# Performance work log

Measured on AMD Instinct MI355X. Metric: run time of the kernel, lower is better.

Reference implementation:

```python
import jax, jax.numpy as jnp
import numpy as np

B, C, H, W = 8, 256, 128, 128
HEADS = 4
HEAD_DIM = C // HEADS  # 64
SCALE = HEAD_DIM ** -0.5


def setup_inputs() -> dict:
    key = jax.random.key(0)
    k1, k2, k3 = jax.random.split(key, 3)
    x = jax.random.normal(k1, (B, C, H, W), dtype=jnp.float32)
    # 1x1 convs == per-pixel linear layers; kaiming-ish small init
    Wqkv = jax.random.normal(k2, (3 * C, C), dtype=jnp.float32) * (1.0 / np.sqrt(C))
    bqkv = jnp.zeros((3 * C,), dtype=jnp.float32)
    Wproj = jax.random.normal(k3, (C, C), dtype=jnp.float32) * (1.0 / np.sqrt(C))
    bproj = jnp.zeros((C,), dtype=jnp.float32)
    return {"x": x, "Wqkv": Wqkv, "bqkv": bqkv, "Wproj": Wproj, "bproj": bproj}


def reference(x, Wqkv, bqkv, Wproj, bproj):
    b, c, h, w = x.shape
    hw = h * w
    xf = x.reshape(b, c, hw)  # [b, c, hw]
    # 1x1 conv QKV projection
    qkv = jnp.einsum('bcn,oc->bon', xf, Wqkv) + bqkv[None, :, None]  # [b, 3c, hw]
    qkv = qkv.reshape(b, 3, HEADS, HEAD_DIM, hw)
    q, k, v = qkv[:, 0], qkv[:, 1], qkv[:, 2]  # each [b, heads, d, hw]
    # channel attention: [b, heads, d, d]
    attn = jnp.einsum('bhdn,bhen->bhde', q, k) * SCALE
    attn = jax.nn.softmax(attn, axis=-1)
    out = jnp.einsum('bhde,bhen->bhdn', attn, v).reshape(b, c, hw)
    # output 1x1 conv
    out = jnp.einsum('bcn,oc->bon', out, Wproj) + bproj[None, :, None]
    return out.reshape(b, c, h, w)
```

## Files before the change

### kernel.cpp

```cpp
#include <hip/hip_runtime.h>
#include <hip/hip_bf16.h>
#include <stdint.h>


#define HW 16384
#define SCALE_F 0.125f
#define NF 16384.0f

typedef __attribute__((ext_vector_type(8))) short bf16x8;
typedef __attribute__((ext_vector_type(4))) float f32x4;

__device__ __forceinline__ unsigned short f2bf(float f) {
    union { float f; uint32_t u; } v; v.f = f;
    uint32_t u = v.u;
    return (unsigned short)((u + 0x7fffu + ((u >> 16) & 1u)) >> 16);
}
__device__ __forceinline__ float bf2f(unsigned short s) {
    union { uint32_t u; float f; } v; v.u = ((uint32_t)s) << 16;
    return v.f;
}

__global__ __launch_bounds__(512) void gram(
        const float* __restrict__ x, float* __restrict__ partG,
        float* __restrict__ parts_s) {
    const int kc = blockIdx.x;
    const int b  = blockIdx.y;
    __shared__ __align__(16) unsigned short Hs[2][256 * 32];
    __shared__ __align__(16) unsigned short Ls[2][256 * 32];
    const int tid = threadIdx.x, lane = tid & 63, w = tid >> 6;
    const int l15 = lane & 15, lg = lane >> 4;
    const int wr = w >> 1, wc = w & 1;
    const int srow = tid >> 1, shalf = tid & 1;
    const int m4 = (srow >> 1) & 3;
    const float* xb = x + (size_t)b * 256 * HW + (size_t)srow * HW + kc * 512 + shalf * 16;
    f32x4 acc[4][8] = {};
    float rs = 0.f;
    float4 ld[4];

#define LOADR(kstep)                                                            \
    {                                                                           \
        const float4* src = reinterpret_cast<const float4*>(xb + (kstep) * 32); \
        ld[0] = src[0]; ld[1] = src[1]; ld[2] = src[2]; ld[3] = src[3];         \
    }
#define STORE(sel)                                                              \
    {                                                                           \
        _Pragma("unroll")                                                       \
        for (int cq = 0; cq < 2; ++cq) {                                        \
            union { unsigned short u[8]; uint4 v; } Hu, Lu;                     \
            const float vv[8] = {ld[2*cq].x, ld[2*cq].y, ld[2*cq].z, ld[2*cq].w,\
                                 ld[2*cq+1].x, ld[2*cq+1].y, ld[2*cq+1].z, ld[2*cq+1].w}; \
            _Pragma("unroll")                                                   \
            for (int i = 0; i < 8; ++i) {                                       \
                Hu.u[i] = f2bf(vv[i]);                                          \
                Lu.u[i] = f2bf(vv[i] - bf2f(Hu.u[i]));                          \
                rs += vv[i];                                                    \
            }                                                                   \
            const int slot = ((shalf * 2 + cq) ^ m4) << 4;                      \
            *reinterpret_cast<uint4*>((char*)(&Hs[sel][0]) + srow * 64 + slot) = Hu.v; \
            *reinterpret_cast<uint4*>((char*)(&Ls[sel][0]) + srow * 64 + slot) = Lu.v; \
        }                                                                       \
    }
#define DO_MFMA(sel)                                                            \
    {                                                                           \
        bf16x8 fah[4], fal[4];                                                  \
        _Pragma("unroll")                                                       \
        for (int i = 0; i < 4; ++i) {                                           \
            const int row = wr * 64 + i * 16 + l15;                             \
            const int off = row * 64 + ((lg ^ ((row >> 1) & 3)) << 4);          \
            fah[i] = *reinterpret_cast<const bf16x8*>((const char*)&Hs[sel][0] + off); \
            fal[i] = *reinterpret_cast<const bf16x8*>((const char*)&Ls[sel][0] + off); \
        }                                                                       \
        _Pragma("unroll")                                                       \
        for (int j = 0; j < 8; ++j) {                                           \
            const int row = wc * 128 + j * 16 + l15;                            \
            const int off = row * 64 + ((lg ^ ((row >> 1) & 3)) << 4);          \
            const bf16x8 fbh = *reinterpret_cast<const bf16x8*>((const char*)&Hs[sel][0] + off); \
            const bf16x8 fbl = *reinterpret_cast<const bf16x8*>((const char*)&Ls[sel][0] + off); \
            _Pragma("unroll")                                                   \
            for (int i = 0; i < 4; ++i) {                                       \
                acc[i][j] = __builtin_amdgcn_mfma_f32_16x16x32_bf16(fah[i], fbh, acc[i][j], 0, 0, 0); \
                acc[i][j] = __builtin_amdgcn_mfma_f32_16x16x32_bf16(fah[i], fbl, acc[i][j], 0, 0, 0); \
                acc[i][j] = __builtin_amdgcn_mfma_f32_16x16x32_bf16(fal[i], fbh, acc[i][j], 0, 0, 0); \
            }                                                                   \
        }                                                                       \
    }

    LOADR(0);
    STORE(0);
    __syncthreads();
    for (int t = 0; t < 16; ++t) {
        if (t < 15) LOADR(t + 1);
        DO_MFMA(t & 1);
        if (t < 15) STORE((t + 1) & 1);
        __syncthreads();
    }
#undef LOADR
#undef STORE
#undef DO_MFMA

    rs += __shfl_xor(rs, 1);
    if ((tid & 1) == 0) parts_s[(size_t)(b * 32 + kc) * 256 + srow] = rs;

    float* pw = partG + (size_t)(b * 32 + kc) * 65536;
    #pragma unroll
    for (int i = 0; i < 4; ++i)
        #pragma unroll
        for (int rr = 0; rr < 4; ++rr) {
            const int m = wr * 64 + i * 16 + lg * 4 + rr;
            #pragma unroll
            for (int j = 0; j < 8; ++j)
                pw[m * 256 + wc * 128 + j * 16 + l15] = acc[i][j][rr];
        }
}

__global__ __launch_bounds__(256) void greduce(
        const float* __restrict__ partG, float* __restrict__ G) {
    const size_t idx = (size_t)blockIdx.x * 256 + threadIdx.x;
    const int b = (int)(idx >> 16);
    const int i = (int)(idx & 65535);
    float sacc = 0.f;
    #pragma unroll
    for (int kc = 0; kc < 32; ++kc)
        sacc += partG[(size_t)(b * 32 + kc) * 65536 + i];
    G[idx] = sacc;
}

__global__ void sreduce(const float* __restrict__ parts_s, float* __restrict__ s) {
    const int b = blockIdx.x, c = threadIdx.x;
    float a = 0.f;
    #pragma unroll
    for (int kc = 0; kc < 32; ++kc)
        a += parts_s[(size_t)(b * 32 + kc) * 256 + c];
    s[b * 256 + c] = a;
}

__global__ __launch_bounds__(256) void tgemm(
        const float* __restrict__ G, const float* __restrict__ Wqkv,
        float* __restrict__ T) {
    const int c0 = blockIdx.x * 64;
    const int d0 = blockIdx.y * 64;
    const int b  = blockIdx.z;
    __shared__ float Ws[64][68];
    __shared__ float Gs[64][68];
    const int tid = threadIdx.x;
    const float* Gb = G + (size_t)b * 65536;
    const int ry = (tid >> 4) * 4, cx = (tid & 15) * 4;
    const int r = tid >> 2, q = (tid & 3) * 16;
    float acc[4][4] = {};

    for (int cb = 0; cb < 4; ++cb) {
        __syncthreads();
        #pragma unroll
        for (int j = 0; j < 16; j += 4) {
            *reinterpret_cast<float4*>(&Ws[r][q + j]) =
                *reinterpret_cast<const float4*>(Wqkv + (size_t)(d0 + r) * 256 + cb * 64 + q + j);
            *reinterpret_cast<float4*>(&Gs[r][q + j]) =
                *reinterpret_cast<const float4*>(Gb + (size_t)(cb * 64 + r) * 256 + c0 + q + j);
        }
        __syncthreads();
        #pragma unroll 8
        for (int k = 0; k < 64; ++k) {
            const float4 g4 = *reinterpret_cast<const float4*>(&Gs[k][cx]);
            #pragma unroll
            for (int i = 0; i < 4; ++i) {
                const float a = Ws[ry + i][k];
                acc[i][0] += a * g4.x;
                acc[i][1] += a * g4.y;
                acc[i][2] += a * g4.z;
                acc[i][3] += a * g4.w;
            }
        }
    }
    float* Tb = T + (size_t)b * 65536;
    #pragma unroll
    for (int i = 0; i < 4; ++i)
        #pragma unroll
        for (int j = 0; j < 4; ++j)
            Tb[(size_t)(d0 + ry + i) * 256 + c0 + cx + j] = acc[i][j];
}

__global__ __launch_bounds__(256) void logits_sm(
        const float* __restrict__ T, const float* __restrict__ Wqkv,
        const float* __restrict__ bqkv, const float* __restrict__ s,
        float* __restrict__ attn) {
    const int bh = blockIdx.x, b = bh >> 2, h = bh & 3;
    const int tid = threadIdx.x;
    __shared__ float Ts[64][257];
    __shared__ float Wks[64][257];
    __shared__ float lgs[64][65];
    __shared__ float qs[64], ks[64];
    const float* Tb = T + (size_t)b * 65536 + (size_t)(h * 64) * 256;
    const float* Wq = Wqkv + (size_t)(h * 64) * 256;
    const float* Wk = Wqkv + (size_t)(256 + h * 64) * 256;

    {
        const int r = tid >> 2, q = (tid & 3) * 64;
        #pragma unroll
        for (int j = 0; j < 64; j += 4) {
            const float4 t4 = *reinterpret_cast<const float4*>(Tb + (size_t)r * 256 + q + j);
            Ts[r][q + j + 0] = t4.x; Ts[r][q + j + 1] = t4.y;
            Ts[r][q + j + 2] = t4.z; Ts[r][q + j + 3] = t4.w;
            const float4 w4 = *reinterpret_cast<const float4*>(Wk + (size_t)r * 256 + q + j);
            Wks[r][q + j + 0] = w4.x; Wks[r][q + j + 1] = w4.y;
            Wks[r][q + j + 2] = w4.z; Wks[r][q + j + 3] = w4.w;
        }
    }
    if (tid < 128) {
        const int d = tid & 63;
        const float* wr = (tid < 64) ? (Wq + (size_t)d * 256) : (Wk + (size_t)d * 256);
        const float* sb = s + b * 256;
        float a = 0.f;
        for (int c = 0; c < 256; ++c) a += wr[c] * sb[c];
        if (tid < 64) qs[d] = a; else ks[d] = a;
    }
    __syncthreads();

    const int d4 = (tid >> 4) * 4, e4 = (tid & 15) * 4;
    float acc[4][4] = {};
    #pragma unroll 4
    for (int c = 0; c < 256; ++c) {
        float tv[4], wv[4];
        #pragma unroll
        for (int i = 0; i < 4; ++i) tv[i] = Ts[d4 + i][c];
        #pragma unroll
        for (int j = 0; j < 4; ++j) wv[j] = Wks[e4 + j][c];
        #pragma unroll
        for (int i = 0; i < 4; ++i)
            #pragma unroll
            for (int j = 0; j < 4; ++j)
                acc[i][j] += tv[i] * wv[j];
    }
    const float* bq = bqkv + h * 64;
    const float* bk = bqkv + 256 + h * 64;
    #pragma unroll
    for (int i = 0; i < 4; ++i) {
        const float bqi = bq[d4 + i], qsi = qs[d4 + i];
        #pragma unroll
        for (int j = 0; j < 4; ++j) {
            const int e = e4 + j;
            lgs[d4 + i][e] = SCALE_F * (acc[i][j] + bqi * ks[e] + bk[e] * qsi + NF * bqi * bk[e]);
        }
    }
    __syncthreads();
    if (tid < 64) {
        float m = -1e30f;
        for (int e = 0; e < 64; ++e) m = fmaxf(m, lgs[tid][e]);
        float sum = 0.f;
        for (int e = 0; e < 64; ++e) {
            const float ex = __expf(lgs[tid][e] - m);
            sum += ex;
            lgs[tid][e] = ex;
        }
        const float inv = 1.f / sum;
        float* ar = attn + ((size_t)bh * 64 + tid) * 64;
        for (int e = 0; e < 64; ++e) ar[e] = lgs[tid][e] * inv;
    }
}

__global__ __launch_bounds__(256) void build_M(
        const float* __restrict__ attn, const float* __restrict__ Wproj,
        float* __restrict__ M) {
    const int g = blockIdx.x * 256 + threadIdx.x;
    const int b = g >> 16, o = (g >> 8) & 255, cpx = g & 255;
    const int h = cpx >> 6, e = cpx & 63;
    const float* wrow = Wproj + (size_t)o * 256 + h * 64;
    const float* acol = attn + ((size_t)(b * 4 + h) * 64) * 64 + e;
    float sacc = 0.f;
    #pragma unroll
    for (int d = 0; d < 64; ++d) sacc += wrow[d] * acol[d * 64];
    M[g] = sacc;
}

__global__ __launch_bounds__(256) void build_P(
        const float* __restrict__ M, const float* __restrict__ Wqkv,
        const float* __restrict__ bqkv, const float* __restrict__ bproj,
        unsigned short* __restrict__ P, float* __restrict__ cvec) {
    const int b = blockIdx.x >> 4, oc = blockIdx.x & 15;
    const int tid = threadIdx.x, c = tid;
    __shared__ float Wvs[32 * 256];
    __shared__ float Ms[16 * 256];
    for (int j = tid; j < 16 * 256; j += 256)
        Ms[j] = M[(size_t)b * 65536 + oc * 16 * 256 + j];
    float acc[16];
    #pragma unroll
    for (int o = 0; o < 16; ++o) acc[o] = 0.f;
    for (int cb2 = 0; cb2 < 8; ++cb2) {
        __syncthreads();
        for (int j = tid; j < 32 * 256; j += 256)
            Wvs[j] = Wqkv[(size_t)(512 + cb2 * 32) * 256 + j];
        __syncthreads();
        for (int c2 = 0; c2 < 32; ++c2) {
            const float wv = Wvs[c2 * 256 + c];
            #pragma unroll
            for (int o = 0; o < 16; ++o)
                acc[o] += Ms[o * 256 + cb2 * 32 + c2] * wv;
        }
    }
    #pragma unroll
    for (int o = 0; o < 16; ++o)
        P[(size_t)b * 65536 + (size_t)(oc * 16 + o) * 256 + c] = f2bf(acc[o]);
    if (tid < 16) {
        const int o = oc * 16 + tid;
        float a = bproj[o];
        for (int c2 = 0; c2 < 256; ++c2)
            a += M[(size_t)b * 65536 + (size_t)o * 256 + c2] * bqkv[512 + c2];
        cvec[b * 256 + o] = a;
    }
}

__global__ __launch_bounds__(512) void out_gemm(
        const unsigned short* __restrict__ P, const float* __restrict__ x,
        const float* __restrict__ cvec, float* __restrict__ out) {
    const int n0 = blockIdx.x * 128;
    const int b  = blockIdx.y;
    __shared__ __align__(16) unsigned short Bs[2][128 * 40];
    const int tid = threadIdx.x, lane = tid & 63, w = tid >> 6;
    const int wr = w >> 1, wc = w & 1;
    const int l15 = lane & 15, lg = lane >> 4;
    const unsigned short* Pb = P + (size_t)b * 65536;
    const float* xb = x + (size_t)b * 256 * HW + n0;
    const int sn = tid & 127, skq = (tid >> 7) * 8;
    f32x4 acc[4][4] = {};
    float bv[8];

#define BLOAD(k0)                                                               \
    {                                                                           \
        _Pragma("unroll")                                                       \
        for (int i = 0; i < 8; ++i)                                             \
            bv[i] = xb[(size_t)((k0) + skq + i) * HW + sn];                     \
    }
#define BSTORE(sel)                                                             \
    {                                                                           \
        union { unsigned short u[8]; uint4 v; } Bu;                             \
        _Pragma("unroll")                                                       \
        for (int i = 0; i < 8; ++i) Bu.u[i] = f2bf(bv[i]);                      \
        *reinterpret_cast<uint4*>(&Bs[sel][sn * 40 + skq]) = Bu.v;              \
    }

    BLOAD(0);
    BSTORE(0);
    __syncthreads();
    for (int t = 0; t < 8; ++t) {
        const int k0 = t * 32;
        if (t < 7) BLOAD(k0 + 32);
        bf16x8 fp[4];
        #pragma unroll
        for (int i = 0; i < 4; ++i)
            fp[i] = *reinterpret_cast<const bf16x8*>(
                Pb + (size_t)(wr * 64 + i * 16 + l15) * 256 + k0 + lg * 8);
        #pragma unroll
        for (int j = 0; j < 4; ++j) {
            const bf16x8 fx = *reinterpret_cast<const bf16x8*>(
                &Bs[t & 1][(wc * 64 + j * 16 + l15) * 40 + lg * 8]);
            #pragma unroll
            for (int i = 0; i < 4; ++i)
                acc[i][j] = __builtin_amdgcn_mfma_f32_16x16x32_bf16(fx, fp[i], acc[i][j], 0, 0, 0);
        }
        if (t < 7) BSTORE((t + 1) & 1);
        __syncthreads();
    }
#undef BLOAD
#undef BSTORE

    float* ob = out + (size_t)b * 256 * HW;
    #pragma unroll
    for (int i = 0; i < 4; ++i) {
        const int m = wr * 64 + i * 16 + l15;
        const float bp = cvec[b * 256 + m];
        #pragma unroll
        for (int j = 0; j < 4; ++j) {
            const int n = n0 + wc * 64 + j * 16 + lg * 4;
            float4 o4;
            o4.x = acc[i][j][0] + bp;
            o4.y = acc[i][j][1] + bp;
            o4.z = acc[i][j][2] + bp;
            o4.w = acc[i][j][3] + bp;
            *reinterpret_cast<float4*>(ob + (size_t)m * HW + n) = o4;
        }
    }
}

extern "C" void kernel_launch(void* const* d_in, const int* in_sizes, int n_in,
                              void* d_out, int out_size, void* d_ws, size_t ws_size,
                              hipStream_t stream) {
    const float* x     = (const float*)d_in[0];
    const float* Wqkv  = (const float*)d_in[1];
    const float* bqkv  = (const float*)d_in[2];
    const float* Wproj = (const float*)d_in[3];
    const float* bproj = (const float*)d_in[4];
    float* out = (float*)d_out;

    char* ws = (char*)d_ws;
    float* partG   = (float*)(ws);
    float* G       = (float*)(ws + 67108864);
    float* attn    = (float*)(ws + 69206016);
    float* M       = (float*)(ws + 69730304);
    unsigned short* P = (unsigned short*)(ws + 71827456);
    float* cvec    = (float*)(ws + 72876032);
    float* s       = (float*)(ws + 72884224);
    float* parts_s = (float*)(ws + 72892416);
    float* T       = (float*)(ws + 73154560);

    gram     <<<dim3(32, 8),   512, 0, stream>>>(x, partG, parts_s);
    greduce  <<<2048,          256, 0, stream>>>(partG, G);
    sreduce  <<<8,             256, 0, stream>>>(parts_s, s);
    tgemm    <<<dim3(4, 4, 8), 256, 0, stream>>>(G, Wqkv, T);
    logits_sm<<<32,            256, 0, stream>>>(T, Wqkv, bqkv, s, attn);
    build_M  <<<2048,          256, 0, stream>>>(attn, Wproj, M);
    build_P  <<<128,           256, 0, stream>>>(M, Wqkv, bqkv, bproj, P, cvec);
    out_gemm <<<dim3(128, 8),  512, 0, stream>>>(P, x, cvec, out);
}
```

Baseline: 233.2 us.

## Stage full x tile into LDS once with XOR swizzle, drop per-step syncs

The out_gemm kernel now loads and converts the whole 256x128 x tile into a 64KB LDS buffer up front, using register double-buffered global loads, then runs all eight K steps of MFMA with no barriers in between. The padded row stride is replaced by an XOR swizzle to avoid LDS bank conflicts. This removes seven __syncthreads and the interleaving of loads with compute, but it gives up overlap of global loads with MFMA work. The larger LDS footprint may also reduce occupancy.

```diff
diff --git a/kernel.cpp b/kernel.cpp
--- a/kernel.cpp
+++ b/kernel.cpp
@@ -313,54 +313,55 @@
         const float* __restrict__ cvec, float* __restrict__ out) {
     const int n0 = blockIdx.x * 128;
     const int b  = blockIdx.y;
-    __shared__ __align__(16) unsigned short Bs[2][128 * 40];
+    __shared__ __align__(16) unsigned short Bs[8 * 128 * 32];
     const int tid = threadIdx.x, lane = tid & 63, w = tid >> 6;
     const int wr = w >> 1, wc = w & 1;
     const int l15 = lane & 15, lg = lane >> 4;
     const unsigned short* Pb = P + (size_t)b * 65536;
-    const float* xb = x + (size_t)b * 256 * HW + n0;
-    const int sn = tid & 127, skq = (tid >> 7) * 8;
+
+    {
+        const int sn = tid & 127;
+        const int sg = tid >> 7;
+        const int wslot = ((sg ^ ((sn >> 1) & 3)) << 4);
+        const float* xcol = x + (size_t)b * 256 * HW + n0 + sn;
+        float bv[2][8];
+        #pragma unroll
+        for (int i = 0; i < 8; ++i)
+            bv[0][i] = xcol[(size_t)(sg * 8 + i) * HW];
+        #pragma unroll
+        for (int s = 0; s < 8; ++s) {
+            if (s < 7) {
+                #pragma unroll
+                for (int i = 0; i < 8; ++i)
+                    bv[(s + 1) & 1][i] = xcol[(size_t)((s + 1) * 32 + sg * 8 + i) * HW];
+            }
+            union { unsigned short u[8]; uint4 v; } Bu;
+            #pragma unroll
+            for (int i = 0; i < 8; ++i) Bu.u[i] = f2bf(bv[s & 1][i]);
+            *reinterpret_cast<uint4*>((char*)Bs + s * 8192 + sn * 64 + wslot) = Bu.v;
+        }
+    }
+    __syncthreads();
+
     f32x4 acc[4][4] = {};
-    float bv[8];
-
-#define BLOAD(k0)                                                               \
-    {                                                                           \
-        _Pragma("unroll")                                                       \
-        for (int i = 0; i < 8; ++i)                                             \
-            bv[i] = xb[(size_t)((k0) + skq + i) * HW + sn];                     \
-    }
-#define BSTORE(sel)                                                             \
-    {                                                                           \
-        union { unsigned short u[8]; uint4 v; } Bu;                             \
-        _Pragma("unroll")                                                       \
-        for (int i = 0; i < 8; ++i) Bu.u[i] = f2bf(bv[i]);                      \
-        *reinterpret_cast<uint4*>(&Bs[sel][sn * 40 + skq]) = Bu.v;              \
-    }
-
-    BLOAD(0);
-    BSTORE(0);
-    __syncthreads();
-    for (int t = 0; t < 8; ++t) {
-        const int k0 = t * 32;
-        if (t < 7) BLOAD(k0 + 32);
+    const int m4r = (l15 >> 1) & 3;
+    #pragma unroll
+    for (int s = 0; s < 8; ++s) {
         bf16x8 fp[4];
         #pragma unroll
         for (int i = 0; i < 4; ++i)
             fp[i] = *reinterpret_cast<const bf16x8*>(
-                Pb + (size_t)(wr * 64 + i * 16 + l15) * 256 + k0 + lg * 8);
+                Pb + (size_t)(wr * 64 + i * 16 + l15) * 256 + s * 32 + lg * 8);
         #pragma unroll
         for (int j = 0; j < 4; ++j) {
+            const int row = wc * 64 + j * 16 + l15;
             const bf16x8 fx = *reinterpret_cast<const bf16x8*>(
-                &Bs[t & 1][(wc * 64 + j * 16 + l15) * 40 + lg * 8]);
+                (const char*)Bs + s * 8192 + row * 64 + ((lg ^ m4r) << 4));
             #pragma unroll
             for (int i = 0; i < 4; ++i)
                 acc[i][j] = __builtin_amdgcn_mfma_f32_16x16x32_bf16(fx, fp[i], acc[i][j], 0, 0, 0);
         }
-        if (t < 7) BSTORE((t + 1) & 1);
-        __syncthreads();
-    }
-#undef BLOAD
-#undef BSTORE
+    }
 
     float* ob = out + (size_t)b * 256 * HW;
     #pragma unroll
```

Result: faster. 227.1 us (-2.6%).
